# Performance work log

Measured on AMD Instinct MI355X. Metric: run time of the kernel, lower is better.

Reference implementation:

```python
import jax, jax.numpy as jnp
import numpy as np

NUM_SYMBOLS = 100000
EMBED_DIM = 256
DIM = 2 * EMBED_DIM          # 512
NUM_HEADS = 4
HEAD_DIM = DIM // NUM_HEADS  # 128
N = 100                      # hard-coded neighbor count in source
EPS = 1e-5


def layernorm(x, g, b):
    mu = jnp.mean(x, axis=-1, keepdims=True)
    var = jnp.var(x, axis=-1, keepdims=True)
    return (x - mu) * jax.lax.rsqrt(var + EPS) * g + b


def setup_inputs() -> dict:
    key = jax.random.key(0)
    ks = jax.random.split(key, 12)
    B, FEW = 512, 2
    connections = jax.random.randint(ks[0], (B, FEW, N, 2), 0, NUM_SYMBOLS)
    mask = jax.random.randint(ks[1], (B * FEW, N, N), 0, 2).astype(jnp.int32)
    s = 0.02
    emb = jax.random.normal(ks[2], (NUM_SYMBOLS + 1, EMBED_DIM), jnp.float32) * s
    qkv_w = jax.random.normal(ks[3], (3 * DIM, DIM), jnp.float32) * s
    qkv_b = jnp.zeros((3 * DIM,), jnp.float32)
    proj_w = jax.random.normal(ks[4], (DIM, DIM), jnp.float32) * s
    proj_b = jnp.zeros((DIM,), jnp.float32)
    ln1_g = jnp.ones((DIM,), jnp.float32); ln1_b = jnp.zeros((DIM,), jnp.float32)
    ln2_g = jnp.ones((DIM,), jnp.float32); ln2_b = jnp.zeros((DIM,), jnp.float32)
    fc_w = jax.random.normal(ks[5], (DIM // 2, DIM), jnp.float32) * s
    fc_b = jnp.zeros((DIM // 2,), jnp.float32)
    return {"connections": connections, "mask": mask, "emb": emb,
            "qkv_w": qkv_w, "qkv_b": qkv_b, "proj_w": proj_w, "proj_b": proj_b,
            "ln1_g": ln1_g, "ln1_b": ln1_b, "ln2_g": ln2_g, "ln2_b": ln2_b,
            "fc_w": fc_w, "fc_b": fc_b}


def reference(connections, mask, emb, qkv_w, qkv_b, proj_w, proj_b,
              ln1_g, ln1_b, ln2_g, ln2_b, fc_w, fc_b):
    # embedding gathers for (relation, entity) pairs
    rel = emb[connections[..., 0]]          # [B, few, N, E]
    ent = emb[connections[..., 1]]          # [B, few, N, E]
    x = jnp.concatenate([rel, ent], axis=-1).reshape(-1, N, DIM)  # [BN, N, C]
    m = mask.reshape(-1, N, N)

    xn = layernorm(x, ln1_g, ln1_b)
    qkv = xn @ qkv_w.T + qkv_b              # [BN, N, 3C]
    BN = xn.shape[0]
    qkv = qkv.reshape(BN, N, 3, NUM_HEADS, HEAD_DIM).transpose(2, 0, 3, 1, 4)
    q, k, v = qkv[0], qkv[1], qkv[2]        # [BN, H, N, hd]

    scale = HEAD_DIM ** -0.5
    attn = jnp.einsum('bhnd,bhmd->bhnm', q, k) * scale
    attn = jnp.where(m[:, None] == 0, -1e9, attn)
    attn = jax.nn.softmax(attn, axis=-1)    # [BN, H, N, N]

    y = jnp.einsum('bhnm,bhmd->bhnd', attn, v)
    y = y.transpose(0, 2, 1, 3).reshape(BN, N, DIM)
    y = y @ proj_w.T + proj_b               # [BN, N, C]

    # attn.mean(dim=2): mean over query axis -> [BN, H, N]; bmm with y
    wc = jnp.einsum('bhn,bnc->bhc', attn.mean(axis=2), y)   # [BN, H, C]
    out = layernorm(wc, ln2_g, ln2_b) @ fc_w.T + fc_b       # [BN, H, C//2]
    return out
```

## Files before the change

kernel.cpp:

```cpp
#include <hip/hip_runtime.h>
#include <stdint.h>

typedef __attribute__((ext_vector_type(8))) short bf16x8;
typedef __attribute__((ext_vector_type(4))) float f32x4;
typedef __attribute__((ext_vector_type(4))) unsigned int u32x4;
typedef __attribute__((ext_vector_type(4))) unsigned short u16x4;

typedef const void __attribute__((address_space(1))) gvoid_t;
typedef void __attribute__((address_space(3))) lvoid_t;

__device__ __forceinline__ unsigned short f2bf(float f) {
  union { float f; unsigned int u; } v; v.f = f;
  unsigned int u = v.u;
  u += 0x7fffu + ((u >> 16) & 1u);
  return (unsigned short)(u >> 16);
}
__device__ __forceinline__ float bf2f(unsigned short h) {
  union { unsigned int u; float f; } v; v.u = ((unsigned int)h) << 16;
  return v.f;
}
__device__ __forceinline__ void load_lds16(const void* g, void* l) {
  __builtin_amdgcn_global_load_lds((gvoid_t*)g, (lvoid_t*)l, 16, 0, 0);
}

__global__ __launch_bounds__(256) void k_cvt(const float* __restrict__ src,
                                             unsigned short* __restrict__ dst, int n) {
  int i = blockIdx.x * 256 + threadIdx.x;
  if (i < n) dst[i] = f2bf(src[i]);
}

__global__ __launch_bounds__(256) void k_gather_ln(const int* __restrict__ conn,
                                                   const float* __restrict__ emb,
                                                   const float* __restrict__ g1,
                                                   const float* __restrict__ b1,
                                                   unsigned short* __restrict__ xn,
                                                   int row0) {
  const int lane = threadIdx.x & 63;
  const int wid = threadIdx.x >> 6;
  const int rloc = blockIdx.x * 4 + wid;
  const int row = row0 + rloc;
  const int rel = conn[row * 2 + 0];
  const int ent = conn[row * 2 + 1];
  const float4 r4 = *(const float4*)(emb + (size_t)rel * 256 + lane * 4);
  const float4 e4 = *(const float4*)(emb + (size_t)ent * 256 + lane * 4);
  float rv[4] = {r4.x, r4.y, r4.z, r4.w};
  float ev[4] = {e4.x, e4.y, e4.z, e4.w};
  float s = 0.f, ss = 0.f;
#pragma unroll
  for (int j = 0; j < 4; ++j) { s += rv[j] + ev[j]; ss += rv[j] * rv[j] + ev[j] * ev[j]; }
#pragma unroll
  for (int d = 1; d < 64; d <<= 1) { s += __shfl_xor(s, d, 64); ss += __shfl_xor(ss, d, 64); }
  const float mu = s * (1.f / 512.f);
  const float var = ss * (1.f / 512.f) - mu * mu;
  const float rs = rsqrtf(var + 1e-5f);
  const float4 ga = *(const float4*)(g1 + lane * 4);
  const float4 gb = *(const float4*)(g1 + 256 + lane * 4);
  const float4 ba = *(const float4*)(b1 + lane * 4);
  const float4 bb = *(const float4*)(b1 + 256 + lane * 4);
  float gav[4] = {ga.x, ga.y, ga.z, ga.w}, gbv[4] = {gb.x, gb.y, gb.z, gb.w};
  float bav[4] = {ba.x, ba.y, ba.z, ba.w}, bbv[4] = {bb.x, bb.y, bb.z, bb.w};
  u16x4 o0, o1;
#pragma unroll
  for (int j = 0; j < 4; ++j) {
    o0[j] = f2bf((rv[j] - mu) * rs * gav[j] + bav[j]);
    o1[j] = f2bf((ev[j] - mu) * rs * gbv[j] + bbv[j]);
  }
  unsigned short* orow = xn + (size_t)rloc * 512;
  *(u16x4*)(orow + lane * 4) = o0;
  *(u16x4*)(orow + 256 + lane * 4) = o1;
}

__global__ __launch_bounds__(256) void k_gemm(const unsigned short* __restrict__ A,
                                              const unsigned short* __restrict__ W,
                                              const float* __restrict__ bias,
                                              unsigned short* __restrict__ C,
                                              int N, int K) {
  __shared__ __align__(16) unsigned short ldsA[2][128 * 32];
  __shared__ __align__(16) unsigned short ldsB[2][128 * 32];
  const int t = threadIdx.x;
  const int lane = t & 63;
  const int wid = t >> 6;
  const int wm = wid >> 1, wn = wid & 1;
  const int mtile = blockIdx.y, ntile = blockIdx.x;
  const size_t Abase = (size_t)mtile * 128 * K;
  const size_t Wbase = (size_t)ntile * 128 * K;
  const int NT = K >> 5;

  f32x4 acc[4][4];
#pragma unroll
  for (int i = 0; i < 4; ++i)
#pragma unroll
    for (int j = 0; j < 4; ++j) acc[i][j] = (f32x4){0.f, 0.f, 0.f, 0.f};

  auto stage = [&](int buf, int kt) {
#pragma unroll
    for (int it = 0; it < 2; ++it) {
      int row = it * 64 + (t >> 2);
      int cl = (t & 3) ^ ((row >> 1) & 3);
      load_lds16(A + Abase + (size_t)row * K + kt * 32 + cl * 8, &ldsA[buf][it * 2048 + t * 8]);
    }
#pragma unroll
    for (int it = 0; it < 2; ++it) {
      int row = it * 64 + (t >> 2);
      int cl = (t & 3) ^ ((row >> 1) & 3);
      load_lds16(W + Wbase + (size_t)row * K + kt * 32 + cl * 8, &ldsB[buf][it * 2048 + t * 8]);
    }
  };

  stage(0, 0);
  __syncthreads();

  for (int kt = 0; kt < NT; ++kt) {
    const int cur = kt & 1;
    if (kt + 1 < NT) stage(cur ^ 1, kt + 1);
    bf16x8 af[4], bfr[4];
#pragma unroll
    for (int mi = 0; mi < 4; ++mi) {
      int row = wm * 64 + mi * 16 + (lane & 15);
      int st = (lane >> 4) ^ ((row >> 1) & 3);
      af[mi] = *(const bf16x8*)&ldsA[cur][row * 32 + st * 8];
    }
#pragma unroll
    for (int ni = 0; ni < 4; ++ni) {
      int row = wn * 64 + ni * 16 + (lane & 15);
      int st = (lane >> 4) ^ ((row >> 1) & 3);
      bfr[ni] = *(const bf16x8*)&ldsB[cur][row * 32 + st * 8];
    }
#pragma unroll
    for (int mi = 0; mi < 4; ++mi)
#pragma unroll
      for (int ni = 0; ni < 4; ++ni)
        acc[mi][ni] = __builtin_amdgcn_mfma_f32_16x16x32_bf16(af[mi], bfr[ni], acc[mi][ni], 0, 0, 0);
    __syncthreads();
  }

#pragma unroll
  for (int ni = 0; ni < 4; ++ni) {
    const int col = ntile * 128 + wn * 64 + ni * 16 + (lane & 15);
    const float bv = bias[col];
#pragma unroll
    for (int mi = 0; mi < 4; ++mi) {
      const int row0 = mtile * 128 + wm * 64 + mi * 16 + ((lane >> 4) << 2);
#pragma unroll
      for (int r = 0; r < 4; ++r)
        C[(size_t)(row0 + r) * N + col] = f2bf(acc[mi][ni][r] + bv);
    }
  }
}

__global__ __launch_bounds__(512) void k_attn(const unsigned short* __restrict__ qkv,
                                              const int* __restrict__ mask,
                                              unsigned short* __restrict__ y,
                                              float* __restrict__ am, int b0) {
  __shared__ __align__(16) unsigned short A_lds[128 * 128];
  __shared__ __align__(16) unsigned short P_lds[7 * 16 * 128];
  __shared__ float am_s[112];
  const int t = threadIdx.x, lane = t & 63, w = t >> 6;
  const int bl = blockIdx.x >> 2, h = blockIdx.x & 3;
  const int bg = b0 + bl;
  const unsigned short* qk = qkv + (size_t)bl * 153600;

  if (t < 112) am_s[t] = 0.f;

#pragma unroll
  for (int j = 0; j < 4; ++j) {
    const int row = j * 32 + w * 4 + (lane >> 4);
    if (row < 100) {
      const int c = (lane & 15) ^ (row & 7);
      load_lds16(qk + (size_t)row * 1536 + 512 + h * 128 + c * 8,
                 &A_lds[j * 4096 + w * 512 + lane * 8]);
    }
  }
  u32x4 vv[4];
#pragma unroll
  for (int p = 0; p < 4; ++p) {
    const int vm = p * 32 + (t >> 4);
    const u32x4 z = {0u, 0u, 0u, 0u};
    vv[p] = (vm < 100) ? *(const u32x4*)(qk + (size_t)vm * 1536 + 1024 + h * 128 + (t & 15) * 8) : z;
  }
  bf16x8 qf[4];
  {
    const int qrow = w * 16 + (lane & 15);
    const bool qv = (w < 7) && (qrow < 100);
#pragma unroll
    for (int kk = 0; kk < 4; ++kk) {
      const bf16x8 z = {0, 0, 0, 0, 0, 0, 0, 0};
      qf[kk] = qv ? *(const bf16x8*)(qk + (size_t)qrow * 1536 + h * 128 + kk * 32 + (lane >> 4) * 8) : z;
    }
  }
  if (t < 192) {
    const u32x4 z = {0u, 0u, 0u, 0u};
    *(u32x4*)&A_lds[(100 + (t >> 4)) * 128 + (t & 15) * 8] = z;
  }
  __syncthreads();

  f32x4 sa[7];
#pragma unroll
  for (int ni = 0; ni < 7; ++ni) sa[ni] = (f32x4){0.f, 0.f, 0.f, 0.f};
  if (w < 7) {
#pragma unroll
    for (int kk = 0; kk < 4; ++kk)
#pragma unroll
      for (int ni = 0; ni < 7; ++ni) {
        const int row = ni * 16 + (lane & 15);
        const int c = (kk * 4 + (lane >> 4)) ^ (row & 7);
        const bf16x8 kf = *(const bf16x8*)&A_lds[row * 128 + (c << 3)];
        sa[ni] = __builtin_amdgcn_mfma_f32_16x16x32_bf16(qf[kk], kf, sa[ni], 0, 0, 0);
      }
  }
  __syncthreads();

#pragma unroll
  for (int p = 0; p < 4; ++p) {
    const int vm = p * 32 + (t >> 4);
    unsigned short tmp[8];
    *(u32x4*)tmp = vv[p];
#pragma unroll
    for (int jj = 0; jj < 8; ++jj) {
      const int d = (lane & 15) * 8 + jj;
      const int swz = (vm >> 3) ^ (((d >> 3) ^ d) & 7);
      A_lds[d * 128 + swz * 8 + (vm & 7)] = tmp[jj];
    }
  }

  if (w < 7) {
    const float scale = 0.08838834764831843f;
    float psum[7] = {0.f, 0.f, 0.f, 0.f, 0.f, 0.f, 0.f};
#pragma unroll
    for (int r = 0; r < 4; ++r) {
      const int lr = (lane >> 4) * 4 + r;
      const int qrow = w * 16 + lr;
      if (qrow < 100) {
        const int* mrow = mask + ((size_t)bg * 100 + qrow) * 100;
        float x[7];
#pragma unroll
        for (int ni = 0; ni < 7; ++ni) {
          const int col = ni * 16 + (lane & 15);
          x[ni] = (col < 100) ? ((mrow[col] == 0) ? -1e9f : sa[ni][r] * scale) : -1e30f;
        }
        float mx = x[0];
#pragma unroll
        for (int ni = 1; ni < 7; ++ni) mx = fmaxf(mx, x[ni]);
#pragma unroll
        for (int dd = 1; dd < 16; dd <<= 1) mx = fmaxf(mx, __shfl_xor(mx, dd, 64));
        float e[7], sum = 0.f;
#pragma unroll
        for (int ni = 0; ni < 7; ++ni) { e[ni] = __expf(x[ni] - mx); sum += e[ni]; }
#pragma unroll
        for (int dd = 1; dd < 16; dd <<= 1) sum += __shfl_xor(sum, dd, 64);
        const float inv = 1.f / sum;
#pragma unroll
        for (int ni = 0; ni < 7; ++ni) {
          const float pv = e[ni] * inv;
          psum[ni] += pv;
          const int col = ni * 16 + (lane & 15);
          const int c = (col >> 3) ^ (lr & 7);
          P_lds[w * 2048 + lr * 128 + c * 8 + (col & 7)] = f2bf(pv);
        }
      } else {
#pragma unroll
        for (int ni = 0; ni < 7; ++ni) {
          const int col = ni * 16 + (lane & 15);
          const int c = (col >> 3) ^ (lr & 7);
          P_lds[w * 2048 + lr * 128 + c * 8 + (col & 7)] = 0;
        }
      }
    }
    if (lane < 32) {
      const int lr = lane & 15;
      const int c = (14 + (lane >> 4)) ^ (lr & 7);
      const u32x4 z = {0u, 0u, 0u, 0u};
      *(u32x4*)&P_lds[w * 2048 + lr * 128 + c * 8] = z;
    }
#pragma unroll
    for (int ni = 0; ni < 7; ++ni) atomicAdd(&am_s[ni * 16 + (lane & 15)], psum[ni]);
  }
  __syncthreads();

  if (t < 100) am[((size_t)bg * 4 + h) * 100 + t] = am_s[t] * 0.01f;

  if (w < 7) {
#pragma unroll
    for (int dt = 0; dt < 8; ++dt) {
      f32x4 acc = {0.f, 0.f, 0.f, 0.f};
#pragma unroll
      for (int kk = 0; kk < 4; ++kk) {
        const int c = kk * 4 + (lane >> 4);
        const bf16x8 pf = *(const bf16x8*)&P_lds[w * 2048 + (lane & 15) * 128 + ((c ^ (lane & 7)) << 3)];
        const int d = dt * 16 + (lane & 15);
        const int cv = c ^ (((d >> 3) ^ d) & 7);
        const bf16x8 vf = *(const bf16x8*)&A_lds[d * 128 + (cv << 3)];
        acc = __builtin_amdgcn_mfma_f32_16x16x32_bf16(pf, vf, acc, 0, 0, 0);
      }
      const int d = dt * 16 + (lane & 15);
#pragma unroll
      for (int r = 0; r < 4; ++r) {
        const int qrow = w * 16 + (lane >> 4) * 4 + r;
        if (qrow < 100)
          y[((size_t)bl * 100 + qrow) * 512 + h * 128 + d] = f2bf(acc[r]);
      }
    }
  }
}

__global__ __launch_bounds__(256) void k_final(const float* __restrict__ am,
                                               const unsigned short* __restrict__ yp,
                                               const float* __restrict__ g2,
                                               const float* __restrict__ b2,
                                               const unsigned short* __restrict__ fcw,
                                               const float* __restrict__ fcb,
                                               float* __restrict__ out, int b0) {
  __shared__ float ams[400];
  __shared__ float wcn[4][512];
  const int b = blockIdx.x, t = threadIdx.x;
  const int bg = b0 + b;
  for (int i = t; i < 400; i += 256) ams[i] = am[(size_t)bg * 400 + i];
  __syncthreads();
  float a0[4] = {0, 0, 0, 0}, a1[4] = {0, 0, 0, 0};
  const unsigned short* yb = yp + (size_t)b * 100 * 512 + t * 2;
  for (int n = 0; n < 100; ++n) {
    const unsigned int u = *(const unsigned int*)(yb + n * 512);
    const float v0 = bf2f((unsigned short)(u & 0xffffu));
    const float v1 = bf2f((unsigned short)(u >> 16));
#pragma unroll
    for (int hh = 0; hh < 4; ++hh) {
      const float ww = ams[hh * 100 + n];
      a0[hh] += ww * v0;
      a1[hh] += ww * v1;
    }
  }
#pragma unroll
  for (int hh = 0; hh < 4; ++hh) {
    wcn[hh][2 * t] = a0[hh];
    wcn[hh][2 * t + 1] = a1[hh];
  }
  __syncthreads();
  {
    const int hh = t >> 6, lane = t & 63;
    float vals[8];
    float s = 0.f, ss = 0.f;
#pragma unroll
    for (int j = 0; j < 8; ++j) {
      const float v = wcn[hh][lane * 8 + j];
      vals[j] = v;
      s += v;
      ss += v * v;
    }
#pragma unroll
    for (int d = 1; d < 64; d <<= 1) { s += __shfl_xor(s, d, 64); ss += __shfl_xor(ss, d, 64); }
    const float mu = s * (1.f / 512.f);
    const float var = ss * (1.f / 512.f) - mu * mu;
    const float rs = rsqrtf(var + 1e-5f);
#pragma unroll
    for (int j = 0; j < 8; ++j) {
      const int c = lane * 8 + j;
      wcn[hh][c] = (vals[j] - mu) * rs * g2[c] + b2[c];
    }
  }
  __syncthreads();
  {
    const int o = t;
    float acc[4] = {0, 0, 0, 0};
    const unsigned short* fr = fcw + (size_t)o * 512;
    for (int c0 = 0; c0 < 512; c0 += 8) {
      unsigned short w8[8];
      *(u32x4*)w8 = *(const u32x4*)(fr + c0);
#pragma unroll
      for (int j = 0; j < 8; ++j) {
        const float wv = bf2f(w8[j]);
#pragma unroll
        for (int hh = 0; hh < 4; ++hh) acc[hh] += wv * wcn[hh][c0 + j];
      }
    }
    const float fb = fcb[o];
#pragma unroll
    for (int hh = 0; hh < 4; ++hh) out[(size_t)bg * 1024 + hh * 256 + o] = acc[hh] + fb;
  }
}

extern "C" void kernel_launch(void* const* d_in, const int* in_sizes, int n_in,
                              void* d_out, int out_size, void* d_ws, size_t ws_size,
                              hipStream_t stream) {
  const int* conn = (const int*)d_in[0];
  const int* mask = (const int*)d_in[1];
  const float* emb = (const float*)d_in[2];
  const float* qkv_w = (const float*)d_in[3];
  const float* qkv_b = (const float*)d_in[4];
  const float* proj_w = (const float*)d_in[5];
  const float* proj_b = (const float*)d_in[6];
  const float* ln1g = (const float*)d_in[7];
  const float* ln1b = (const float*)d_in[8];
  const float* ln2g = (const float*)d_in[9];
  const float* ln2b = (const float*)d_in[10];
  const float* fc_w = (const float*)d_in[11];
  const float* fc_b = (const float*)d_in[12];
  float* out = (float*)d_out;

  size_t off = 0;
  auto alloc = [&](size_t bytes) {
    void* p = (char*)d_ws + off;
    off += (bytes + 255) & ~(size_t)255;
    return p;
  };
  unsigned short* w_qkv = (unsigned short*)alloc((size_t)1536 * 512 * 2);
  unsigned short* w_proj = (unsigned short*)alloc((size_t)512 * 512 * 2);
  unsigned short* w_fc = (unsigned short*)alloc((size_t)256 * 512 * 2);
  float* am = (float*)alloc((size_t)1024 * 400 * 4);
  const size_t fixed = off;

  int CB = 1024;
  while (CB > 32) {
    size_t need = fixed + (size_t)CB * 100 * 512 * 2 + (size_t)CB * 100 * 1536 * 2 + 1024;
    if (need <= ws_size) break;
    CB >>= 1;
  }
  unsigned short* xn = (unsigned short*)alloc((size_t)CB * 100 * 512 * 2);
  unsigned short* qkvb = (unsigned short*)alloc((size_t)CB * 100 * 1536 * 2);

  k_cvt<<<(786432 + 255) / 256, 256, 0, stream>>>(qkv_w, w_qkv, 786432);
  k_cvt<<<(262144 + 255) / 256, 256, 0, stream>>>(proj_w, w_proj, 262144);
  k_cvt<<<(131072 + 255) / 256, 256, 0, stream>>>(fc_w, w_fc, 131072);

  const int mt = CB * 100 / 128;
  for (int b0 = 0; b0 < 1024; b0 += CB) {
    k_gather_ln<<<CB * 25, 256, 0, stream>>>(conn, emb, ln1g, ln1b, xn, b0 * 100);
    k_gemm<<<dim3(12, mt), 256, 0, stream>>>(xn, w_qkv, qkv_b, qkvb, 1536, 512);
    k_attn<<<CB * 4, 512, 0, stream>>>(qkvb, mask, xn , am, b0);
    k_gemm<<<dim3(4, mt), 256, 0, stream>>>(xn , w_proj, proj_b, qkvb , 512, 512);
    k_final<<<CB, 256, 0, stream>>>(am, qkvb , ln2g, ln2b, w_fc, fc_b, out, b0);
  }
}
```

Before: 636.9 us.

## Replace GEMM with 256x256-tile, 8-wave pipelined kernel using XCD-aware block remap

Replaces the 128x128, 4-wave bf16 GEMM with a 256x256-tile, 512-thread kernel. It splits each 64-wide K step into four phases, interleaving LDS reads, async global-to-LDS staging and MFMA groups. Phases are ordered with explicit waitcnt and barriers and raise wave priority around the MFMAs. Block indices are remapped so consecutive tiles stay on the same XCD, and the MFMA operands are swapped so each lane writes four packed bf16 outputs in one store. The goals are more operand reuse per LDS byte, better L2 locality and fewer store instructions. The cost is higher register and LDS pressure, and the minimum chunk size rises to 64 so row counts divide by 256.

Result: slower. 661.6 us (+3.9%).

```diff
diff --git a/kernel.cpp b/kernel.cpp
--- a/kernel.cpp
+++ b/kernel.cpp
@@ -22,6 +22,15 @@
 __device__ __forceinline__ void load_lds16(const void* g, void* l) {
   __builtin_amdgcn_global_load_lds((gvoid_t*)g, (lvoid_t*)l, 16, 0, 0);
 }
+
+#define GATE4() asm volatile("s_waitcnt vmcnt(4)" ::: "memory")
+#define LGKM0() asm volatile("s_waitcnt lgkmcnt(0)" ::: "memory")
+#define BARRIER()                          \
+  do {                                     \
+    asm volatile("" ::: "memory");         \
+    __builtin_amdgcn_s_barrier();          \
+    asm volatile("" ::: "memory");         \
+  } while (0)
 
 __global__ __launch_bounds__(256) void k_cvt(const float* __restrict__ src,
                                              unsigned short* __restrict__ dst, int n) {
@@ -70,80 +79,119 @@
   *(u16x4*)(orow + 256 + lane * 4) = o1;
 }
 
-__global__ __launch_bounds__(256) void k_gemm(const unsigned short* __restrict__ A,
-                                              const unsigned short* __restrict__ W,
-                                              const float* __restrict__ bias,
-                                              unsigned short* __restrict__ C,
-                                              int N, int K) {
-  __shared__ __align__(16) unsigned short ldsA[2][128 * 32];
-  __shared__ __align__(16) unsigned short ldsB[2][128 * 32];
-  const int t = threadIdx.x;
-  const int lane = t & 63;
-  const int wid = t >> 6;
-  const int wm = wid >> 1, wn = wid & 1;
-  const int mtile = blockIdx.y, ntile = blockIdx.x;
-  const size_t Abase = (size_t)mtile * 128 * K;
-  const size_t Wbase = (size_t)ntile * 128 * K;
-  const int NT = K >> 5;
-
-  f32x4 acc[4][4];
-#pragma unroll
-  for (int i = 0; i < 4; ++i)
+__global__ __launch_bounds__(512, 2) void k_gemm2(const unsigned short* __restrict__ A,
+                                                  const unsigned short* __restrict__ W,
+                                                  const float* __restrict__ bias,
+                                                  unsigned short* __restrict__ C,
+                                                  int N, int K, int ntiles, int nwg) {
+  __shared__ __align__(16) unsigned short ldsA[2][2][256 * 32];
+  __shared__ __align__(16) unsigned short ldsB[2][2][256 * 32];
+
+  const int orig = blockIdx.x;
+  const int q = nwg >> 3, r = nwg & 7;
+  const int xcd = orig & 7, idx = orig >> 3;
+  const int wg = (xcd < r ? xcd * (q + 1) : r * (q + 1) + (xcd - r) * q) + idx;
+  const int mtile = wg / ntiles, ntile = wg % ntiles;
+
+  const int t = threadIdx.x, lane = t & 63, w = t >> 6;
+  const int wm = w >> 2, wn = w & 3;
+  const size_t Abase = (size_t)mtile * 256 * K;
+  const size_t Wbase = (size_t)ntile * 256 * K;
+  const int NIT = K >> 6;
+
+  const int sr = t >> 2;
+  const int sc = (t & 3) ^ ((sr >> 1) & 3);
+
+  auto stageA = [&](int buf, int kk, int kt2) {
+    const unsigned short* s = A + Abase + (size_t)sr * K + kt2 * 64 + kk * 32 + sc * 8;
+    unsigned short* d = &ldsA[buf][kk][t * 8];
+    load_lds16(s, d);
+    load_lds16(s + (size_t)128 * K, d + 4096);
+  };
+  auto stageB = [&](int buf, int kk, int kt2) {
+    const unsigned short* s = W + Wbase + (size_t)sr * K + kt2 * 64 + kk * 32 + sc * 8;
+    unsigned short* d = &ldsB[buf][kk][t * 8];
+    load_lds16(s, d);
+    load_lds16(s + (size_t)128 * K, d + 4096);
+  };
+
+  f32x4 acc[8][4];
+#pragma unroll
+  for (int i = 0; i < 8; ++i)
 #pragma unroll
     for (int j = 0; j < 4; ++j) acc[i][j] = (f32x4){0.f, 0.f, 0.f, 0.f};
 
-  auto stage = [&](int buf, int kt) {
-#pragma unroll
-    for (int it = 0; it < 2; ++it) {
-      int row = it * 64 + (t >> 2);
-      int cl = (t & 3) ^ ((row >> 1) & 3);
-      load_lds16(A + Abase + (size_t)row * K + kt * 32 + cl * 8, &ldsA[buf][it * 2048 + t * 8]);
-    }
-#pragma unroll
-    for (int it = 0; it < 2; ++it) {
-      int row = it * 64 + (t >> 2);
-      int cl = (t & 3) ^ ((row >> 1) & 3);
-      load_lds16(W + Wbase + (size_t)row * K + kt * 32 + cl * 8, &ldsB[buf][it * 2048 + t * 8]);
-    }
-  };
-
-  stage(0, 0);
-  __syncthreads();
-
-  for (int kt = 0; kt < NT; ++kt) {
-    const int cur = kt & 1;
-    if (kt + 1 < NT) stage(cur ^ 1, kt + 1);
-    bf16x8 af[4], bfr[4];
-#pragma unroll
-    for (int mi = 0; mi < 4; ++mi) {
-      int row = wm * 64 + mi * 16 + (lane & 15);
-      int st = (lane >> 4) ^ ((row >> 1) & 3);
-      af[mi] = *(const bf16x8*)&ldsA[cur][row * 32 + st * 8];
-    }
-#pragma unroll
-    for (int ni = 0; ni < 4; ++ni) {
-      int row = wn * 64 + ni * 16 + (lane & 15);
-      int st = (lane >> 4) ^ ((row >> 1) & 3);
-      bfr[ni] = *(const bf16x8*)&ldsB[cur][row * 32 + st * 8];
-    }
-#pragma unroll
-    for (int mi = 0; mi < 4; ++mi)
-#pragma unroll
-      for (int ni = 0; ni < 4; ++ni)
-        acc[mi][ni] = __builtin_amdgcn_mfma_f32_16x16x32_bf16(af[mi], bfr[ni], acc[mi][ni], 0, 0, 0);
-    __syncthreads();
+  bf16x8 af[8], br[2];
+
+  auto readA = [&](int buf, int kk) {
+#pragma unroll
+    for (int mi = 0; mi < 8; ++mi) {
+      const int row = wm * 128 + mi * 16 + (lane & 15);
+      const int c = (lane >> 4) ^ ((row >> 1) & 3);
+      af[mi] = *(const bf16x8*)&ldsA[buf][kk][row * 32 + c * 8];
+    }
+  };
+  auto readB2 = [&](int buf, int kk, int nh) {
+#pragma unroll
+    for (int ni = 0; ni < 2; ++ni) {
+      const int row = wn * 64 + (nh * 2 + ni) * 16 + (lane & 15);
+      const int c = (lane >> 4) ^ ((row >> 1) & 3);
+      br[ni] = *(const bf16x8*)&ldsB[buf][kk][row * 32 + c * 8];
+    }
+  };
+  auto quad = [&](int nh) {
+#pragma unroll
+    for (int mi = 0; mi < 8; ++mi)
+#pragma unroll
+      for (int ni = 0; ni < 2; ++ni)
+        acc[mi][nh * 2 + ni] =
+            __builtin_amdgcn_mfma_f32_16x16x32_bf16(br[ni], af[mi], acc[mi][nh * 2 + ni], 0, 0, 0);
+  };
+
+  stageA(0, 0, 0); stageB(0, 0, 0); stageA(0, 1, 0); stageB(0, 1, 0);
+  GATE4();
+  BARRIER();
+
+  for (int kt = 0; kt < NIT; ++kt) {
+    const int cur = kt & 1, nxt = cur ^ 1;
+    const int ktn = (kt + 1 < NIT) ? kt + 1 : 0;
+    readA(cur, 0); readB2(cur, 0, 0);
+    stageA(nxt, 0, ktn);
+    BARRIER(); LGKM0();
+    __builtin_amdgcn_s_setprio(1); quad(0); __builtin_amdgcn_s_setprio(0);
+    BARRIER();
+    readB2(cur, 0, 1);
+    stageB(nxt, 0, ktn);
+    BARRIER(); LGKM0();
+    __builtin_amdgcn_s_setprio(1); quad(1); __builtin_amdgcn_s_setprio(0);
+    GATE4();
+    BARRIER();
+    readA(cur, 1); readB2(cur, 1, 0);
+    stageA(nxt, 1, ktn);
+    BARRIER(); LGKM0();
+    __builtin_amdgcn_s_setprio(1); quad(0); __builtin_amdgcn_s_setprio(0);
+    BARRIER();
+    readB2(cur, 1, 1);
+    stageB(nxt, 1, ktn);
+    BARRIER(); LGKM0();
+    __builtin_amdgcn_s_setprio(1); quad(1); __builtin_amdgcn_s_setprio(0);
+    GATE4();
+    BARRIER();
   }
 
 #pragma unroll
   for (int ni = 0; ni < 4; ++ni) {
-    const int col = ntile * 128 + wn * 64 + ni * 16 + (lane & 15);
-    const float bv = bias[col];
-#pragma unroll
-    for (int mi = 0; mi < 4; ++mi) {
-      const int row0 = mtile * 128 + wm * 64 + mi * 16 + ((lane >> 4) << 2);
-#pragma unroll
-      for (int r = 0; r < 4; ++r)
-        C[(size_t)(row0 + r) * N + col] = f2bf(acc[mi][ni][r] + bv);
+    const int colb = ntile * 256 + wn * 64 + ni * 16 + ((lane >> 4) << 2);
+    const float4 bv = *(const float4*)(bias + colb);
+#pragma unroll
+    for (int mi = 0; mi < 8; ++mi) {
+      const int row = mtile * 256 + wm * 128 + mi * 16 + (lane & 15);
+      const unsigned int lo =
+          (unsigned int)f2bf(acc[mi][ni][0] + bv.x) | ((unsigned int)f2bf(acc[mi][ni][1] + bv.y) << 16);
+      const unsigned int hi =
+          (unsigned int)f2bf(acc[mi][ni][2] + bv.z) | ((unsigned int)f2bf(acc[mi][ni][3] + bv.w) << 16);
+      uint2 pk; pk.x = lo; pk.y = hi;
+      *(uint2*)(C + (size_t)row * N + colb) = pk;
     }
   }
 }
@@ -409,7 +457,7 @@
   const size_t fixed = off;
 
   int CB = 1024;
-  while (CB > 32) {
+  while (CB > 64) {
     size_t need = fixed + (size_t)CB * 100 * 512 * 2 + (size_t)CB * 100 * 1536 * 2 + 1024;
     if (need <= ws_size) break;
     CB >>= 1;
@@ -421,12 +469,14 @@
   k_cvt<<<(262144 + 255) / 256, 256, 0, stream>>>(proj_w, w_proj, 262144);
   k_cvt<<<(131072 + 255) / 256, 256, 0, stream>>>(fc_w, w_fc, 131072);
 
-  const int mt = CB * 100 / 128;
+  const int mtiles = CB * 100 / 256;
+  const int nwg_qkv = 6 * mtiles;
+  const int nwg_proj = 2 * mtiles;
   for (int b0 = 0; b0 < 1024; b0 += CB) {
     k_gather_ln<<<CB * 25, 256, 0, stream>>>(conn, emb, ln1g, ln1b, xn, b0 * 100);
-    k_gemm<<<dim3(12, mt), 256, 0, stream>>>(xn, w_qkv, qkv_b, qkvb, 1536, 512);
+    k_gemm2<<<nwg_qkv, 512, 0, stream>>>(xn, w_qkv, qkv_b, qkvb, 1536, 512, 6, nwg_qkv);
     k_attn<<<CB * 4, 512, 0, stream>>>(qkvb, mask, xn , am, b0);
-    k_gemm<<<dim3(4, mt), 256, 0, stream>>>(xn , w_proj, proj_b, qkvb , 512, 512);
+    k_gemm2<<<nwg_proj, 512, 0, stream>>>(xn , w_proj, proj_b, qkvb , 512, 512, 2, nwg_proj);
     k_final<<<CB, 256, 0, stream>>>(am, qkvb , ln2g, ln2b, w_fc, fc_b, out, b0);
   }
 }
```

## Reorder projection after attention-mean reduction, pack mask bits, triple-buffer GEMM

Applied to the files above, without the earlier changes.

Attention-mean weights are applied to the attention output before the output projection rather than after it. This shrinks the projection GEMM from every token row to four rows per batch item; because the mean weights sum to one, the bias still passes through unchanged. LN2 and the final FC become a small norm kernel plus the same GEMM with float output. The int32 mask is packed into per-row bitmasks by a separate kernel so the attention kernel reads 16 bytes per row, and the GEMM moves to a 3-stage LDS pipeline with explicit vmcnt gating and an XCD-aware block remap. The trade-offs are extra kernel launches, a bf16 rounding of the intermediate before projection, and a smaller chunk size.

After: 546.8 us. -14.1%, faster.

```diff
diff --git a/kernel.cpp b/kernel.cpp
--- a/kernel.cpp
+++ b/kernel.cpp
@@ -23,10 +23,41 @@
   __builtin_amdgcn_global_load_lds((gvoid_t*)g, (lvoid_t*)l, 16, 0, 0);
 }
 
+#define GATE4() asm volatile("s_waitcnt vmcnt(4)" ::: "memory")
+#define GATE0() asm volatile("s_waitcnt vmcnt(0)" ::: "memory")
+#define BARRIER()                    \
+  do {                               \
+    asm volatile("" ::: "memory");   \
+    __builtin_amdgcn_s_barrier();    \
+    asm volatile("" ::: "memory");   \
+  } while (0)
+
 __global__ __launch_bounds__(256) void k_cvt(const float* __restrict__ src,
                                              unsigned short* __restrict__ dst, int n) {
   int i = blockIdx.x * 256 + threadIdx.x;
   if (i < n) dst[i] = f2bf(src[i]);
+}
+
+__global__ __launch_bounds__(256) void k_maskpack(const int* __restrict__ mask,
+                                                  unsigned int* __restrict__ bm) {
+  const int lane = threadIdx.x & 63;
+  const int wv = (blockIdx.x << 2) + (threadIdx.x >> 6);
+  const int r0 = wv * 16;
+  for (int i = 0; i < 16; ++i) {
+    const int r = r0 + i;
+    const size_t base = (size_t)r * 100;
+    const int c0 = mask[base + lane];
+    int c1 = 0;
+    if (lane < 36) c1 = mask[base + 64 + lane];
+    const unsigned long long b0 = __ballot(c0 != 0);
+    const unsigned long long b1 = __ballot(c1 != 0);
+    if (lane == 0) {
+      u32x4 v;
+      v[0] = (unsigned int)b0; v[1] = (unsigned int)(b0 >> 32);
+      v[2] = (unsigned int)b1; v[3] = (unsigned int)(b1 >> 32);
+      *(u32x4*)(bm + (size_t)r * 4) = v;
+    }
+  }
 }
 
 __global__ __launch_bounds__(256) void k_gather_ln(const int* __restrict__ conn,
@@ -70,18 +101,23 @@
   *(u16x4*)(orow + 256 + lane * 4) = o1;
 }
 
-__global__ __launch_bounds__(256) void k_gemm(const unsigned short* __restrict__ A,
-                                              const unsigned short* __restrict__ W,
-                                              const float* __restrict__ bias,
-                                              unsigned short* __restrict__ C,
-                                              int N, int K) {
-  __shared__ __align__(16) unsigned short ldsA[2][128 * 32];
-  __shared__ __align__(16) unsigned short ldsB[2][128 * 32];
-  const int t = threadIdx.x;
-  const int lane = t & 63;
-  const int wid = t >> 6;
+template <typename CT>
+__global__ __launch_bounds__(256) void k_gemm3(const unsigned short* __restrict__ A,
+                                               const unsigned short* __restrict__ W,
+                                               const float* __restrict__ bias,
+                                               CT* __restrict__ C,
+                                               int N, int K, int ntiles, int nwg) {
+  __shared__ __align__(16) unsigned short ldsA[3][128 * 32];
+  __shared__ __align__(16) unsigned short ldsB[3][128 * 32];
+
+  const int orig = blockIdx.x;
+  const int q = nwg >> 3, r = nwg & 7;
+  const int xcd = orig & 7, idx = orig >> 3;
+  const int wg = (xcd < r ? xcd * (q + 1) : r * (q + 1) + (xcd - r) * q) + idx;
+  const int mtile = wg / ntiles, ntile = wg % ntiles;
+
+  const int t = threadIdx.x, lane = t & 63, wid = t >> 6;
   const int wm = wid >> 1, wn = wid & 1;
-  const int mtile = blockIdx.y, ntile = blockIdx.x;
   const size_t Abase = (size_t)mtile * 128 * K;
   const size_t Wbase = (size_t)ntile * 128 * K;
   const int NT = K >> 5;
@@ -92,38 +128,44 @@
 #pragma unroll
     for (int j = 0; j < 4; ++j) acc[i][j] = (f32x4){0.f, 0.f, 0.f, 0.f};
 
+  const int sr0 = t >> 2;
   auto stage = [&](int buf, int kt) {
 #pragma unroll
     for (int it = 0; it < 2; ++it) {
-      int row = it * 64 + (t >> 2);
-      int cl = (t & 3) ^ ((row >> 1) & 3);
+      const int row = it * 64 + sr0;
+      const int cl = (t & 3) ^ ((row >> 1) & 3);
       load_lds16(A + Abase + (size_t)row * K + kt * 32 + cl * 8, &ldsA[buf][it * 2048 + t * 8]);
     }
 #pragma unroll
     for (int it = 0; it < 2; ++it) {
-      int row = it * 64 + (t >> 2);
-      int cl = (t & 3) ^ ((row >> 1) & 3);
+      const int row = it * 64 + sr0;
+      const int cl = (t & 3) ^ ((row >> 1) & 3);
       load_lds16(W + Wbase + (size_t)row * K + kt * 32 + cl * 8, &ldsB[buf][it * 2048 + t * 8]);
     }
   };
 
   stage(0, 0);
-  __syncthreads();
-
+  stage(1, 1);
+
+  int cur = 0;
   for (int kt = 0; kt < NT; ++kt) {
-    const int cur = kt & 1;
-    if (kt + 1 < NT) stage(cur ^ 1, kt + 1);
+    if (kt + 1 < NT) { GATE4(); } else { GATE0(); }
+    BARRIER();
+    if (kt + 2 < NT) {
+      int s2 = cur + 2; if (s2 >= 3) s2 -= 3;
+      stage(s2, kt + 2);
+    }
     bf16x8 af[4], bfr[4];
 #pragma unroll
     for (int mi = 0; mi < 4; ++mi) {
-      int row = wm * 64 + mi * 16 + (lane & 15);
-      int st = (lane >> 4) ^ ((row >> 1) & 3);
+      const int row = wm * 64 + mi * 16 + (lane & 15);
+      const int st = (lane >> 4) ^ ((row >> 1) & 3);
       af[mi] = *(const bf16x8*)&ldsA[cur][row * 32 + st * 8];
     }
 #pragma unroll
     for (int ni = 0; ni < 4; ++ni) {
-      int row = wn * 64 + ni * 16 + (lane & 15);
-      int st = (lane >> 4) ^ ((row >> 1) & 3);
+      const int row = wn * 64 + ni * 16 + (lane & 15);
+      const int st = (lane >> 4) ^ ((row >> 1) & 3);
       bfr[ni] = *(const bf16x8*)&ldsB[cur][row * 32 + st * 8];
     }
 #pragma unroll
@@ -131,7 +173,7 @@
 #pragma unroll
       for (int ni = 0; ni < 4; ++ni)
         acc[mi][ni] = __builtin_amdgcn_mfma_f32_16x16x32_bf16(af[mi], bfr[ni], acc[mi][ni], 0, 0, 0);
-    __syncthreads();
+    cur = (cur + 1 == 3) ? 0 : cur + 1;
   }
 
 #pragma unroll
@@ -142,14 +184,19 @@
     for (int mi = 0; mi < 4; ++mi) {
       const int row0 = mtile * 128 + wm * 64 + mi * 16 + ((lane >> 4) << 2);
 #pragma unroll
-      for (int r = 0; r < 4; ++r)
-        C[(size_t)(row0 + r) * N + col] = f2bf(acc[mi][ni][r] + bv);
+      for (int r2 = 0; r2 < 4; ++r2) {
+        const float ov = acc[mi][ni][r2] + bv;
+        if constexpr (sizeof(CT) == 2)
+          C[(size_t)(row0 + r2) * N + col] = (CT)f2bf(ov);
+        else
+          C[(size_t)(row0 + r2) * N + col] = (CT)ov;
+      }
     }
   }
 }
 
 __global__ __launch_bounds__(512) void k_attn(const unsigned short* __restrict__ qkv,
-                                              const int* __restrict__ mask,
+                                              const unsigned int* __restrict__ bm,
                                               unsigned short* __restrict__ y,
                                               float* __restrict__ am, int b0) {
   __shared__ __align__(16) unsigned short A_lds[128 * 128];
@@ -231,12 +278,13 @@
       const int lr = (lane >> 4) * 4 + r;
       const int qrow = w * 16 + lr;
       if (qrow < 100) {
-        const int* mrow = mask + ((size_t)bg * 100 + qrow) * 100;
+        const u32x4 bmv = *(const u32x4*)(bm + ((size_t)bg * 100 + qrow) * 4);
         float x[7];
 #pragma unroll
         for (int ni = 0; ni < 7; ++ni) {
           const int col = ni * 16 + (lane & 15);
-          x[ni] = (col < 100) ? ((mrow[col] == 0) ? -1e9f : sa[ni][r] * scale) : -1e30f;
+          const unsigned int bit = (bmv[ni >> 1] >> (((ni & 1) << 4) + (lane & 15))) & 1u;
+          x[ni] = (col < 100) ? (bit ? sa[ni][r] * scale : -1e9f) : -1e30f;
         }
         float mx = x[0];
 #pragma unroll
@@ -303,23 +351,18 @@
   }
 }
 
-__global__ __launch_bounds__(256) void k_final(const float* __restrict__ am,
-                                               const unsigned short* __restrict__ yp,
-                                               const float* __restrict__ g2,
-                                               const float* __restrict__ b2,
-                                               const unsigned short* __restrict__ fcw,
-                                               const float* __restrict__ fcb,
-                                               float* __restrict__ out, int b0) {
+__global__ __launch_bounds__(256) void k_z(const float* __restrict__ am,
+                                           const unsigned short* __restrict__ y,
+                                           unsigned short* __restrict__ zb, int b0) {
   __shared__ float ams[400];
-  __shared__ float wcn[4][512];
-  const int b = blockIdx.x, t = threadIdx.x;
-  const int bg = b0 + b;
+  const int bl = blockIdx.x, t = threadIdx.x;
+  const int bg = b0 + bl;
   for (int i = t; i < 400; i += 256) ams[i] = am[(size_t)bg * 400 + i];
   __syncthreads();
   float a0[4] = {0, 0, 0, 0}, a1[4] = {0, 0, 0, 0};
-  const unsigned short* yb = yp + (size_t)b * 100 * 512 + t * 2;
+  const unsigned short* yb = y + (size_t)bl * 100 * 512 + t * 2;
   for (int n = 0; n < 100; ++n) {
-    const unsigned int u = *(const unsigned int*)(yb + n * 512);
+    const unsigned int u = *(const unsigned int*)(yb + (size_t)n * 512);
     const float v0 = bf2f((unsigned short)(u & 0xffffu));
     const float v1 = bf2f((unsigned short)(u >> 16));
 #pragma unroll
@@ -331,51 +374,46 @@
   }
 #pragma unroll
   for (int hh = 0; hh < 4; ++hh) {
-    wcn[hh][2 * t] = a0[hh];
-    wcn[hh][2 * t + 1] = a1[hh];
-  }
-  __syncthreads();
-  {
-    const int hh = t >> 6, lane = t & 63;
-    float vals[8];
-    float s = 0.f, ss = 0.f;
-#pragma unroll
-    for (int j = 0; j < 8; ++j) {
-      const float v = wcn[hh][lane * 8 + j];
-      vals[j] = v;
-      s += v;
-      ss += v * v;
-    }
-#pragma unroll
-    for (int d = 1; d < 64; d <<= 1) { s += __shfl_xor(s, d, 64); ss += __shfl_xor(ss, d, 64); }
-    const float mu = s * (1.f / 512.f);
-    const float var = ss * (1.f / 512.f) - mu * mu;
-    const float rs = rsqrtf(var + 1e-5f);
-#pragma unroll
-    for (int j = 0; j < 8; ++j) {
-      const int c = lane * 8 + j;
-      wcn[hh][c] = (vals[j] - mu) * rs * g2[c] + b2[c];
-    }
-  }
-  __syncthreads();
-  {
-    const int o = t;
-    float acc[4] = {0, 0, 0, 0};
-    const unsigned short* fr = fcw + (size_t)o * 512;
-    for (int c0 = 0; c0 < 512; c0 += 8) {
-      unsigned short w8[8];
-      *(u32x4*)w8 = *(const u32x4*)(fr + c0);
-#pragma unroll
-      for (int j = 0; j < 8; ++j) {
-        const float wv = bf2f(w8[j]);
-#pragma unroll
-        for (int hh = 0; hh < 4; ++hh) acc[hh] += wv * wcn[hh][c0 + j];
-      }
-    }
-    const float fb = fcb[o];
-#pragma unroll
-    for (int hh = 0; hh < 4; ++hh) out[(size_t)bg * 1024 + hh * 256 + o] = acc[hh] + fb;
-  }
+    const unsigned int pk = (unsigned int)f2bf(a0[hh]) | ((unsigned int)f2bf(a1[hh]) << 16);
+    *(unsigned int*)(zb + ((size_t)(bl * 4 + hh)) * 512 + 2 * t) = pk;
+  }
+}
+
+__global__ __launch_bounds__(256) void k_ln2(const unsigned short* __restrict__ wcb,
+                                             const float* __restrict__ g2,
+                                             const float* __restrict__ b2,
+                                             unsigned short* __restrict__ wcn) {
+  const int t = threadIdx.x, lane = t & 63, w = t >> 6;
+  const int row = blockIdx.x * 4 + w;
+  const u32x4 pv = *(const u32x4*)(wcb + (size_t)row * 512 + lane * 8);
+  float v[8];
+#pragma unroll
+  for (int j = 0; j < 4; ++j) {
+    v[2 * j] = bf2f((unsigned short)(pv[j] & 0xffffu));
+    v[2 * j + 1] = bf2f((unsigned short)(pv[j] >> 16));
+  }
+  float s = 0.f, ss = 0.f;
+#pragma unroll
+  for (int j = 0; j < 8; ++j) { s += v[j]; ss += v[j] * v[j]; }
+#pragma unroll
+  for (int d = 1; d < 64; d <<= 1) { s += __shfl_xor(s, d, 64); ss += __shfl_xor(ss, d, 64); }
+  const float mu = s * (1.f / 512.f);
+  const float var = ss * (1.f / 512.f) - mu * mu;
+  const float rs = rsqrtf(var + 1e-5f);
+  const float4 ga = *(const float4*)(g2 + lane * 8);
+  const float4 gb = *(const float4*)(g2 + lane * 8 + 4);
+  const float4 ba = *(const float4*)(b2 + lane * 8);
+  const float4 bb = *(const float4*)(b2 + lane * 8 + 4);
+  const float gv[8] = {ga.x, ga.y, ga.z, ga.w, gb.x, gb.y, gb.z, gb.w};
+  const float bv[8] = {ba.x, ba.y, ba.z, ba.w, bb.x, bb.y, bb.z, bb.w};
+  u32x4 ov;
+#pragma unroll
+  for (int j = 0; j < 4; ++j) {
+    const unsigned short lo = f2bf((v[2 * j] - mu) * rs * gv[2 * j] + bv[2 * j]);
+    const unsigned short hi = f2bf((v[2 * j + 1] - mu) * rs * gv[2 * j + 1] + bv[2 * j + 1]);
+    ov[j] = (unsigned int)lo | ((unsigned int)hi << 16);
+  }
+  *(u32x4*)(wcn + (size_t)row * 512 + lane * 8) = ov;
 }
 
 extern "C" void kernel_launch(void* const* d_in, const int* in_sizes, int n_in,
@@ -406,27 +444,36 @@
   unsigned short* w_proj = (unsigned short*)alloc((size_t)512 * 512 * 2);
   unsigned short* w_fc = (unsigned short*)alloc((size_t)256 * 512 * 2);
   float* am = (float*)alloc((size_t)1024 * 400 * 4);
+  unsigned int* bmb = (unsigned int*)alloc((size_t)102400 * 16);
   const size_t fixed = off;
 
-  int CB = 1024;
-  while (CB > 32) {
-    size_t need = fixed + (size_t)CB * 100 * 512 * 2 + (size_t)CB * 100 * 1536 * 2 + 1024;
+  int CB = 512;
+  while (CB > 64) {
+    size_t need = fixed + (size_t)CB * 4 * 512 * 2 * 3 + (size_t)CB * 100 * 512 * 2 +
+                  (size_t)CB * 100 * 1536 * 2 + 4096;
     if (need <= ws_size) break;
     CB >>= 1;
   }
+  unsigned short* zbuf = (unsigned short*)alloc((size_t)CB * 4 * 512 * 2);
+  unsigned short* wcb = (unsigned short*)alloc((size_t)CB * 4 * 512 * 2);
+  unsigned short* wcn = (unsigned short*)alloc((size_t)CB * 4 * 512 * 2);
   unsigned short* xn = (unsigned short*)alloc((size_t)CB * 100 * 512 * 2);
   unsigned short* qkvb = (unsigned short*)alloc((size_t)CB * 100 * 1536 * 2);
 
   k_cvt<<<(786432 + 255) / 256, 256, 0, stream>>>(qkv_w, w_qkv, 786432);
   k_cvt<<<(262144 + 255) / 256, 256, 0, stream>>>(proj_w, w_proj, 262144);
   k_cvt<<<(131072 + 255) / 256, 256, 0, stream>>>(fc_w, w_fc, 131072);
-
-  const int mt = CB * 100 / 128;
+  k_maskpack<<<1600, 256, 0, stream>>>(mask, bmb);
+
   for (int b0 = 0; b0 < 1024; b0 += CB) {
+    const int mt = CB * 100 / 128;
+    const int zt = CB * 4 / 128;
     k_gather_ln<<<CB * 25, 256, 0, stream>>>(conn, emb, ln1g, ln1b, xn, b0 * 100);
-    k_gemm<<<dim3(12, mt), 256, 0, stream>>>(xn, w_qkv, qkv_b, qkvb, 1536, 512);
-    k_attn<<<CB * 4, 512, 0, stream>>>(qkvb, mask, xn , am, b0);
-    k_gemm<<<dim3(4, mt), 256, 0, stream>>>(xn , w_proj, proj_b, qkvb , 512, 512);
-    k_final<<<CB, 256, 0, stream>>>(am, qkvb , ln2g, ln2b, w_fc, fc_b, out, b0);
-  }
-}
+    k_gemm3<unsigned short><<<12 * mt, 256, 0, stream>>>(xn, w_qkv, qkv_b, qkvb, 1536, 512, 12, 12 * mt);
+    k_attn<<<CB * 4, 512, 0, stream>>>(qkvb, bmb, xn , am, b0);
+    k_z<<<CB, 256, 0, stream>>>(am, xn , zbuf, b0);
+    k_gemm3<unsigned short><<<4 * zt, 256, 0, stream>>>(zbuf, w_proj, proj_b, wcb, 512, 512, 4, 4 * zt);
+    k_ln2<<<CB, 256, 0, stream>>>(wcb, ln2g, ln2b, wcn);
+    k_gemm3<float><<<2 * zt, 256, 0, stream>>>(wcn, w_fc, fc_b, out + (size_t)b0 * 1024, 256, 512, 2, 2 * zt);
+  }
+}
```
